# Optimization experiments

Measured on AMD Instinct MI355X. Metric: run time of the kernel, lower is better.

The kernel has to match this reference:

```python
import jax, jax.numpy as jnp
import numpy as np

PATCH_LEN = 16
PATCH_STRIDE = 8
DIM = 512
NUM_HEADS = 8
HEAD_DIM = DIM // NUM_HEADS
NUM_LAYERS = 4
MLP_HIDDEN = 4 * DIM
ROPE_BASE = 10000.0
LN_EPS = 1e-5


def setup_inputs() -> dict:
    key = jax.random.key(0)
    ks = jax.random.split(key, 20)
    B, T, C = 4, 8192, 7
    s = 0.02
    inp = {
        "x": jax.random.normal(ks[0], (B, T, C), dtype=jnp.float32),
        "W_emb": jax.random.normal(ks[1], (PATCH_LEN * C, DIM), dtype=jnp.float32) * s,
        "b_emb": jnp.zeros((DIM,), jnp.float32),
        "ln1_g": jnp.ones((NUM_LAYERS, DIM), jnp.float32),
        "ln1_b": jnp.zeros((NUM_LAYERS, DIM), jnp.float32),
        "W_qkv": jax.random.normal(ks[2], (NUM_LAYERS, DIM, 3 * DIM), dtype=jnp.float32) * s,
        "b_qkv": jnp.zeros((NUM_LAYERS, 3 * DIM), jnp.float32),
        "W_proj": jax.random.normal(ks[3], (NUM_LAYERS, DIM, DIM), dtype=jnp.float32) * s,
        "b_proj": jnp.zeros((NUM_LAYERS, DIM), jnp.float32),
        "ln2_g": jnp.ones((NUM_LAYERS, DIM), jnp.float32),
        "ln2_b": jnp.zeros((NUM_LAYERS, DIM), jnp.float32),
        "W_mlp1": jax.random.normal(ks[4], (NUM_LAYERS, DIM, MLP_HIDDEN), dtype=jnp.float32) * s,
        "b_mlp1": jnp.zeros((NUM_LAYERS, MLP_HIDDEN), jnp.float32),
        "W_mlp2": jax.random.normal(ks[5], (NUM_LAYERS, MLP_HIDDEN, DIM), dtype=jnp.float32) * s,
        "b_mlp2": jnp.zeros((NUM_LAYERS, DIM), jnp.float32),
        "lnf_g": jnp.ones((DIM,), jnp.float32),
        "lnf_b": jnp.zeros((DIM,), jnp.float32),
    }
    return inp


def _layer_norm(x, g, b):
    mu = jnp.mean(x, axis=-1, keepdims=True)
    var = jnp.mean(jnp.square(x - mu), axis=-1, keepdims=True)
    return (x - mu) * jax.lax.rsqrt(var + LN_EPS) * g + b


def _rotate_half(x):
    x1, x2 = jnp.split(x, 2, axis=-1)
    return jnp.concatenate((-x2, x1), axis=-1)


def _rope_cos_sin(seq_len):
    t = jnp.arange(seq_len, dtype=jnp.float32)
    inv_freq = 1.0 / (ROPE_BASE ** (jnp.arange(0, HEAD_DIM, 2, dtype=jnp.float32) / HEAD_DIM))
    freqs = jnp.outer(t, inv_freq)                      # [L, hd/2]
    emb = jnp.concatenate((freqs, freqs), axis=-1)      # [L, hd]
    return jnp.cos(emb), jnp.sin(emb)


def _forward(x, W_emb, b_emb, ln1_g, ln1_b, W_qkv, b_qkv, W_proj, b_proj,
             ln2_g, ln2_b, W_mlp1, b_mlp1, W_mlp2, b_mlp2, lnf_g, lnf_b):
    B, T, C = x.shape
    n = (T - PATCH_LEN) // PATCH_STRIDE + 1
    # torch unfold: [B, n, C, patch_len], then flattened as (C, patch_len)
    idx = jnp.arange(n)[:, None] * PATCH_STRIDE + jnp.arange(PATCH_LEN)[None, :]  # [n, P]
    patches = x[:, idx, :]                              # [B, n, P, C]
    patches = patches.transpose(0, 1, 3, 2).reshape(B, n, C * PATCH_LEN)
    emb = patches @ W_emb + b_emb                       # [B, n, D]

    cos, sin = _rope_cos_sin(n)                         # [n, hd]
    cos = cos[None, None, :, :]
    sin = sin[None, None, :, :]
    scale = HEAD_DIM ** -0.5

    h = emb
    for i in range(NUM_LAYERS):
        # --- attention ---
        y = _layer_norm(h, ln1_g[i], ln1_b[i])
        qkv = (y @ W_qkv[i] + b_qkv[i]).reshape(B, n, 3, NUM_HEADS, HEAD_DIM)
        qkv = qkv.transpose(2, 0, 3, 1, 4)              # [3, B, H, n, hd]
        q, k, v = qkv[0], qkv[1], qkv[2]
        q = q * cos + _rotate_half(q) * sin
        k = k * cos + _rotate_half(k) * sin
        attn = jax.nn.softmax(jnp.einsum('bhqd,bhkd->bhqk', q, k) * scale, axis=-1)
        o = jnp.einsum('bhqk,bhkd->bhqd', attn, v)      # [B, H, n, hd]
        o = o.transpose(0, 2, 1, 3).reshape(B, n, DIM)
        h = h + (o @ W_proj[i] + b_proj[i])
        # --- mlp ---
        y = _layer_norm(h, ln2_g[i], ln2_b[i])
        y = jax.nn.gelu(y @ W_mlp1[i] + b_mlp1[i], approximate=False)
        h = h + (y @ W_mlp2[i] + b_mlp2[i])

    x_out = _layer_norm(h, lnf_g, lnf_b)
    return emb, x_out


def reference(x, W_emb, b_emb, ln1_g, ln1_b, W_qkv, b_qkv, W_proj, b_proj,
              ln2_g, ln2_b, W_mlp1, b_mlp1, W_mlp2, b_mlp2, lnf_g, lnf_b):
    return _forward(x, W_emb, b_emb, ln1_g, ln1_b, W_qkv, b_qkv, W_proj, b_proj,
                    ln2_g, ln2_b, W_mlp1, b_mlp1, W_mlp2, b_mlp2, lnf_g, lnf_b)
```

## Files before the change

### kernel.cpp

```cpp
#include <hip/hip_runtime.h>
#include <hip/hip_bf16.h>
#include <math.h>

#define B_SZ 4
#define T_LEN 8192
#define C_IN 7
#define NPATCH 1023
#define DIM 512
#define NH 8
#define HD 64
#define NLAYERS 4
#define MLP_HID 2048
#define M_ROWS (B_SZ * NPATCH)
#define KEMB 128
#define LN_EPS 1e-5f

typedef __attribute__((ext_vector_type(8))) short short8;
typedef __attribute__((ext_vector_type(4))) float float4v;

static __device__ __forceinline__ unsigned short f2bf(float f) {
  __hip_bfloat16 h = __float2bfloat16(f);
  return *reinterpret_cast<unsigned short*>(&h);
}
static __device__ __forceinline__ float bf2f(unsigned short u) {
  return __uint_as_float(((unsigned)u) << 16);
}

__global__ __launch_bounds__(256) void patch_kernel(
    const float* __restrict__ x, unsigned short* __restrict__ Pm) {
  int idx = blockIdx.x * 256 + threadIdx.x;
  if (idx >= M_ROWS * KEMB) return;
  int row = idx >> 7, c = idx & 127;
  float v = 0.f;
  if (c < 112) {
    int b = row / NPATCH, i = row - b * NPATCH;
    int ci = c >> 4, p = c & 15;
    v = x[((size_t)b * T_LEN + (size_t)i * 8 + p) * C_IN + ci];
  }
  Pm[idx] = f2bf(v);
}

__global__ __launch_bounds__(256) void wemb_cvt_kernel(
    const float* __restrict__ W, unsigned short* __restrict__ Wt) {
  int idx = blockIdx.x * 256 + threadIdx.x;
  if (idx >= DIM * KEMB) return;
  int n = idx >> 7, k = idx & 127;
  float v = (k < 112) ? W[(size_t)k * DIM + n] : 0.f;
  Wt[idx] = f2bf(v);
}

template <bool BF>
__global__ __launch_bounds__(256) void ln_kernel(
    const float* __restrict__ in, const float* __restrict__ g,
    const float* __restrict__ bb, void* __restrict__ outv, int M) {
  int row = blockIdx.x * 4 + (threadIdx.x >> 6);
  if (row >= M) return;
  int lane = threadIdx.x & 63;
  const float* xr = in + (size_t)row * DIM;
  float v[8];
  float s = 0.f;
  #pragma unroll
  for (int k = 0; k < 8; ++k) { v[k] = xr[lane + 64 * k]; s += v[k]; }
  #pragma unroll
  for (int off = 32; off; off >>= 1) s += __shfl_down(s, off);
  s = __shfl(s, 0);
  float mu = s * (1.f / DIM);
  float q = 0.f;
  #pragma unroll
  for (int k = 0; k < 8; ++k) { float d = v[k] - mu; q = fmaf(d, d, q); }
  #pragma unroll
  for (int off = 32; off; off >>= 1) q += __shfl_down(q, off);
  q = __shfl(q, 0);
  float rstd = rsqrtf(q * (1.f / DIM) + LN_EPS);
  #pragma unroll
  for (int k = 0; k < 8; ++k) {
    int d = lane + 64 * k;
    float r = (v[k] - mu) * rstd * g[d] + bb[d];
    if (BF)
      ((unsigned short*)outv)[(size_t)row * DIM + d] = f2bf(r);
    else
      ((float*)outv)[(size_t)row * DIM + d] = r;
  }
}

__global__ __launch_bounds__(256) void wcvt_kernel(
    const float* __restrict__ W, unsigned short* __restrict__ Wt, int K, int N) {
  __shared__ float tile[32][33];
  int n0 = blockIdx.x * 32, k0 = blockIdx.y * 32, L = blockIdx.z;
  const float* Ws = W + (size_t)L * K * N;
  unsigned short* Wd = Wt + (size_t)L * K * N;
  int tx = threadIdx.x & 31, ty = threadIdx.x >> 5;
  #pragma unroll
  for (int i = 0; i < 4; ++i)
    tile[ty + i * 8][tx] = Ws[(size_t)(k0 + ty + i * 8) * N + n0 + tx];
  __syncthreads();
  #pragma unroll
  for (int i = 0; i < 4; ++i)
    Wd[(size_t)(n0 + ty + i * 8) * K + k0 + tx] = f2bf(tile[tx][ty + i * 8]);
}

__global__ __launch_bounds__(256) void rope_tab_kernel(float2* __restrict__ tab) {
  int idx = blockIdx.x * 256 + threadIdx.x;
  if (idx >= NPATCH * 32) return;
  int i = idx >> 5, j = idx & 31;
  float inv = powf(10000.0f, -(float)j * (1.0f / 32.0f));
  float sn, cs;
  sincosf((float)i * inv, &sn, &cs);
  tab[idx] = make_float2(cs, sn);
}

template <int TM, int TN, int EPI>
__global__ __launch_bounds__(256) void mfma_gemm(
    const unsigned short* __restrict__ A, const unsigned short* __restrict__ Bt,
    const float* __restrict__ bias, const float* __restrict__ res,
    float* __restrict__ Cf, float* __restrict__ Cf2,
    unsigned short* __restrict__ Cb, const float2* __restrict__ rtab,
    int M, int N, int K) {
  constexpr int WM = TM / 2, WN = TN / 2;
  constexpr int NI = WM / 16, NJ = WN / 16;
  constexpr int ACH = TM * 4;
  constexpr int TCH = (TM + TN) * 4;
  constexpr int CH = TCH / 256;
  __shared__ __align__(16) unsigned short As[2][TM][40];
  __shared__ __align__(16) unsigned short Bs[2][TN][40];
  const int bm = blockIdx.y * TM;
  const int bn = blockIdx.x * TN;
  const int tid = threadIdx.x;
  const int lane = tid & 63, wave = tid >> 6;
  const int quad = lane >> 4, l16 = lane & 15;
  const int wm = (wave & 1) * WM;
  const int wn = (wave >> 1) * WN;

  float4v acc[NI][NJ];
  #pragma unroll
  for (int i = 0; i < NI; ++i)
    #pragma unroll
    for (int j = 0; j < NJ; ++j)
      acc[i][j] = (float4v){0.f, 0.f, 0.f, 0.f};

  uint4 pr[CH];
  auto load_regs = [&](int kk) {
    #pragma unroll
    for (int it = 0; it < CH; ++it) {
      int c = tid + it * 256;
      if (c < ACH) {
        int row = c >> 2, ch = (c & 3) * 8;
        int gm = bm + row;
        pr[it] = make_uint4(0u, 0u, 0u, 0u);
        if (gm < M) pr[it] = *(const uint4*)(A + (size_t)gm * K + kk + ch);
      } else {
        int c2 = c - ACH;
        int row = c2 >> 2, ch = (c2 & 3) * 8;
        pr[it] = *(const uint4*)(Bt + (size_t)(bn + row) * K + kk + ch);
      }
    }
  };

  load_regs(0);
  int buf = 0;
  for (int k0 = 0; k0 < K; k0 += 32, buf ^= 1) {
    #pragma unroll
    for (int it = 0; it < CH; ++it) {
      int c = tid + it * 256;
      if (c < ACH)
        *(uint4*)&As[buf][c >> 2][(c & 3) * 8] = pr[it];
      else {
        int c2 = c - ACH;
        *(uint4*)&Bs[buf][c2 >> 2][(c2 & 3) * 8] = pr[it];
      }
    }
    if (k0 + 32 < K) load_regs(k0 + 32);
    __syncthreads();
    short8 af[NI], bfr[NJ];
    #pragma unroll
    for (int i = 0; i < NI; ++i)
      af[i] = *(const short8*)&As[buf][wm + i * 16 + l16][quad * 8];
    #pragma unroll
    for (int j = 0; j < NJ; ++j)
      bfr[j] = *(const short8*)&Bs[buf][wn + j * 16 + l16][quad * 8];
    #pragma unroll
    for (int i = 0; i < NI; ++i)
      #pragma unroll
      for (int j = 0; j < NJ; ++j)
        acc[i][j] = __builtin_amdgcn_mfma_f32_16x16x32_bf16(
            af[i], bfr[j], acc[i][j], 0, 0, 0);
  }

  if (EPI == 6) {
    const int sec = (bn + wn) >> 9;
    #pragma unroll
    for (int i = 0; i < NI; ++i) {
      int gm0 = bm + wm + i * 16 + quad * 4;
      #pragma unroll
      for (int r = 0; r < 4; ++r) {
        int gm = gm0 + r;
        if (gm >= M) continue;
        size_t rowoff = (size_t)gm * N;
        if (sec < 2) {
          int ip = gm; if (ip >= 2046) ip -= 2046; if (ip >= 1023) ip -= 1023;
          float sc = (sec == 0) ? 0.125f : 1.f;
          #pragma unroll
          for (int j = 0; j < 2; ++j) {
            int gn = bn + wn + j * 16 + l16;
            float v0 = acc[i][j][r] + bias[gn];
            float v1 = acc[i][j + 2][r] + bias[gn + 32];
            float2 t = rtab[ip * 32 + j * 16 + l16];
            Cb[rowoff + gn]      = f2bf((v0 * t.x - v1 * t.y) * sc);
            Cb[rowoff + gn + 32] = f2bf((v1 * t.x + v0 * t.y) * sc);
          }
        } else {
          #pragma unroll
          for (int j = 0; j < 4; ++j) {
            int gn = bn + wn + j * 16 + l16;
            Cb[rowoff + gn] = f2bf(acc[i][j][r] + bias[gn]);
          }
        }
      }
    }
    return;
  }

  #pragma unroll
  for (int j = 0; j < NJ; ++j) {
    int gn = bn + wn + j * 16 + l16;
    float bv = bias[gn];
    #pragma unroll
    for (int i = 0; i < NI; ++i) {
      int gm0 = bm + wm + i * 16 + quad * 4;
      #pragma unroll
      for (int r = 0; r < 4; ++r) {
        int gm = gm0 + r;
        if (gm < M) {
          float v = acc[i][j][r] + bv;
          size_t off = (size_t)gm * N + gn;
          if (EPI == 1) {
            Cf[off] = v + res[off];
          } else if (EPI == 2) {
            Cb[off] = f2bf(0.5f * v * (1.f + erff(v * 0.70710678118f)));
          } else if (EPI == 3) {
            Cb[off] = f2bf(v);
          } else {
            Cf[off] = v;
            Cf2[off] = v;
          }
        }
      }
    }
  }
}

#define APITCH 72

__global__ __launch_bounds__(256) void attn_kernel(
    const unsigned short* __restrict__ qkvb, unsigned short* __restrict__ o) {
  const int qt0 = blockIdx.x * 64;
  const int h = blockIdx.y;
  const int b = blockIdx.z;
  const int tid = threadIdx.x;
  const int lane = tid & 63, wave = tid >> 6;
  const int quad = lane >> 4, l16 = lane & 15;

  __shared__ __align__(16) unsigned short Qs[64][APITCH];
  __shared__ __align__(16) unsigned short Vt[2][HD][APITCH];
  __shared__ __align__(16) unsigned short Ps[4][16][APITCH];

  const int sr = tid >> 2;
  const int sc0 = (tid & 3) * 16;
  {
    int qi = qt0 + sr;
    uint4 a = make_uint4(0u, 0u, 0u, 0u), b2 = a;
    if (qi < NPATCH) {
      const uint4* src = (const uint4*)(qkvb + (size_t)(b * NPATCH + qi) * (3 * DIM) + h * HD + sc0);
      a = src[0]; b2 = src[1];
    }
    *(uint4*)&Qs[sr][sc0] = a;
    *(uint4*)&Qs[sr][sc0 + 8] = b2;
  }

  const int kp = tid & 31, dg = tid >> 5;
  uint4 pv0, pv1;
  auto load_v = [&](int j0) {
    pv0 = pv1 = make_uint4(0u, 0u, 0u, 0u);
    int j = j0 + 2 * kp;
    const unsigned short* vb = qkvb + (size_t)(b * NPATCH + j) * (3 * DIM) + 2 * DIM + h * HD + dg * 8;
    if (j < NPATCH)     pv0 = *(const uint4*)vb;
    if (j + 1 < NPATCH) pv1 = *(const uint4*)(vb + 3 * DIM);
  };

  const unsigned short* kbase = qkvb + (size_t)b * NPATCH * (3 * DIM) + DIM + (size_t)h * HD;
  uint4 nk0[4], nk1[4];
  auto load_k = [&](int j0) {
    #pragma unroll
    for (int j = 0; j < 4; ++j) {
      int row = j0 + j * 16 + l16;
      nk0[j] = make_uint4(0u, 0u, 0u, 0u);
      nk1[j] = nk0[j];
      if (row < NPATCH) {
        const uint4* kr = (const uint4*)(kbase + (size_t)row * (3 * DIM) + quad * 8);
        nk0[j] = kr[0];
        nk1[j] = kr[4];
      }
    }
  };

  load_v(0);
  load_k(0);
  __syncthreads();

  short8 aq0 = *(const short8*)&Qs[wave * 16 + l16][quad * 8];
  short8 aq1 = *(const short8*)&Qs[wave * 16 + l16][32 + quad * 8];

  float4v accO[4];
  #pragma unroll
  for (int j2 = 0; j2 < 4; ++j2) accO[j2] = (float4v){0.f, 0.f, 0.f, 0.f};
  float m_run[4] = {-1e30f, -1e30f, -1e30f, -1e30f};
  float lp[4] = {0.f, 0.f, 0.f, 0.f};

  int buf = 0;
  for (int j0 = 0; j0 < NPATCH; j0 += 64, buf ^= 1) {
    {
      unsigned short va[8], vb8[8];
      *(uint4*)&va[0] = pv0;
      *(uint4*)&vb8[0] = pv1;
      #pragma unroll
      for (int u = 0; u < 8; ++u) {
        unsigned pk = (unsigned)va[u] | ((unsigned)vb8[u] << 16);
        *(unsigned*)&Vt[buf][dg * 8 + u][2 * kp] = pk;
      }
    }
    __syncthreads();

    float4v s[4];
    __builtin_amdgcn_s_setprio(1);
    #pragma unroll
    for (int j = 0; j < 4; ++j) {
      s[j] = (float4v){0.f, 0.f, 0.f, 0.f};
      s[j] = __builtin_amdgcn_mfma_f32_16x16x32_bf16(
          aq0, __builtin_bit_cast(short8, nk0[j]), s[j], 0, 0, 0);
      s[j] = __builtin_amdgcn_mfma_f32_16x16x32_bf16(
          aq1, __builtin_bit_cast(short8, nk1[j]), s[j], 0, 0, 0);
    }
    __builtin_amdgcn_s_setprio(0);

    if (j0 + 64 < NPATCH) { load_k(j0 + 64); load_v(j0 + 64); }

    float mx[4];
    #pragma unroll
    for (int r = 0; r < 4; ++r)
      mx[r] = fmaxf(fmaxf(s[0][r], s[1][r]), fmaxf(s[2][r], s[3][r]));
    #pragma unroll
    for (int mask = 1; mask < 16; mask <<= 1)
      #pragma unroll
      for (int r = 0; r < 4; ++r)
        mx[r] = fmaxf(mx[r], __shfl_xor(mx[r], mask));
    float g = fmaxf(fmaxf(mx[0] - m_run[0], mx[1] - m_run[1]),
                    fmaxf(mx[2] - m_run[2], mx[3] - m_run[3]));
    if (!__all(g <= 8.f)) {
      #pragma unroll
      for (int r = 0; r < 4; ++r) {
        float mnew = fmaxf(m_run[r], mx[r]);
        float al = __expf(m_run[r] - mnew);
        m_run[r] = mnew;
        lp[r] *= al;
        #pragma unroll
        for (int j2 = 0; j2 < 4; ++j2) accO[j2][r] *= al;
      }
    }
    #pragma unroll
    for (int j = 0; j < 4; ++j) {
      bool valid = (j0 + j * 16 + l16) < NPATCH;
      #pragma unroll
      for (int r = 0; r < 4; ++r) {
        float p = valid ? __expf(s[j][r] - m_run[r]) : 0.f;
        lp[r] += p;
        Ps[wave][quad * 4 + r][j * 16 + l16] = f2bf(p);
      }
    }

    short8 pa0 = *(const short8*)&Ps[wave][l16][quad * 8];
    short8 pa1 = *(const short8*)&Ps[wave][l16][32 + quad * 8];
    __builtin_amdgcn_s_setprio(1);
    #pragma unroll
    for (int j2 = 0; j2 < 4; ++j2) {
      short8 v0 = *(const short8*)&Vt[buf][j2 * 16 + l16][quad * 8];
      short8 v1 = *(const short8*)&Vt[buf][j2 * 16 + l16][32 + quad * 8];
      accO[j2] = __builtin_amdgcn_mfma_f32_16x16x32_bf16(pa0, v0, accO[j2], 0, 0, 0);
      accO[j2] = __builtin_amdgcn_mfma_f32_16x16x32_bf16(pa1, v1, accO[j2], 0, 0, 0);
    }
    __builtin_amdgcn_s_setprio(0);
  }

  #pragma unroll
  for (int mask = 1; mask < 16; mask <<= 1)
    #pragma unroll
    for (int r = 0; r < 4; ++r)
      lp[r] += __shfl_xor(lp[r], mask);

  #pragma unroll
  for (int r = 0; r < 4; ++r) {
    int qi = qt0 + wave * 16 + quad * 4 + r;
    if (qi < NPATCH) {
      float inv = 1.f / lp[r];
      size_t off = (size_t)(b * NPATCH + qi) * DIM + h * HD + l16;
      #pragma unroll
      for (int j2 = 0; j2 < 4; ++j2)
        o[off + j2 * 16] = f2bf(accO[j2][r] * inv);
    }
  }
}

extern "C" void kernel_launch(void* const* d_in, const int* in_sizes, int n_in,
                              void* d_out, int out_size, void* d_ws, size_t ws_size,
                              hipStream_t stream) {
  const float* x      = (const float*)d_in[0];
  const float* W_emb  = (const float*)d_in[1];
  const float* b_emb  = (const float*)d_in[2];
  const float* ln1_g  = (const float*)d_in[3];
  const float* ln1_b  = (const float*)d_in[4];
  const float* W_qkv  = (const float*)d_in[5];
  const float* b_qkv  = (const float*)d_in[6];
  const float* W_proj = (const float*)d_in[7];
  const float* b_proj = (const float*)d_in[8];
  const float* ln2_g  = (const float*)d_in[9];
  const float* ln2_b  = (const float*)d_in[10];
  const float* W_mlp1 = (const float*)d_in[11];
  const float* b_mlp1 = (const float*)d_in[12];
  const float* W_mlp2 = (const float*)d_in[13];
  const float* b_mlp2 = (const float*)d_in[14];
  const float* lnf_g  = (const float*)d_in[15];
  const float* lnf_b  = (const float*)d_in[16];
  float* out = (float*)d_out;

  float* h              = (float*)d_ws;
  unsigned short* qkvb  = (unsigned short*)(h + (size_t)M_ROWS * DIM);
  unsigned short* midbf = qkvb;
  unsigned short* ybf   = qkvb + (size_t)M_ROWS * MLP_HID;
  unsigned short* obf   = ybf;
  unsigned short* wqkv_t  = ybf + (size_t)M_ROWS * DIM;
  unsigned short* wproj_t = wqkv_t  + (size_t)NLAYERS * DIM * 3 * DIM;
  unsigned short* wmlp1_t = wproj_t + (size_t)NLAYERS * DIM * DIM;
  unsigned short* wmlp2_t = wmlp1_t + (size_t)NLAYERS * DIM * MLP_HID;
  float2* rtab = (float2*)(wmlp2_t + (size_t)NLAYERS * MLP_HID * DIM);
  unsigned short* Pm    = (unsigned short*)(rtab + (size_t)NPATCH * 32);
  unsigned short* Wembt = Pm + (size_t)M_ROWS * KEMB;

  wcvt_kernel<<<dim3(3 * DIM / 32, DIM / 32, NLAYERS), 256, 0, stream>>>(W_qkv,  wqkv_t,  DIM, 3 * DIM);
  wcvt_kernel<<<dim3(DIM / 32, DIM / 32, NLAYERS),     256, 0, stream>>>(W_proj, wproj_t, DIM, DIM);
  wcvt_kernel<<<dim3(MLP_HID / 32, DIM / 32, NLAYERS), 256, 0, stream>>>(W_mlp1, wmlp1_t, DIM, MLP_HID);
  wcvt_kernel<<<dim3(DIM / 32, MLP_HID / 32, NLAYERS), 256, 0, stream>>>(W_mlp2, wmlp2_t, MLP_HID, DIM);
  rope_tab_kernel<<<(NPATCH * 32 + 255) / 256, 256, 0, stream>>>(rtab);
  patch_kernel<<<(M_ROWS * KEMB + 255) / 256, 256, 0, stream>>>(x, Pm);
  wemb_cvt_kernel<<<(DIM * KEMB + 255) / 256, 256, 0, stream>>>(W_emb, Wembt);

  const int MT64 = (M_ROWS + 63) / 64;
  const int LNG = (M_ROWS + 3) / 4;

  mfma_gemm<64, 64, 5><<<dim3(DIM / 64, MT64), 256, 0, stream>>>(
      Pm, Wembt, b_emb, nullptr, out, h, nullptr, nullptr, M_ROWS, DIM, KEMB);

  for (int L = 0; L < NLAYERS; ++L) {
    ln_kernel<true><<<LNG, 256, 0, stream>>>(h, ln1_g + L * DIM, ln1_b + L * DIM, ybf, M_ROWS);
    mfma_gemm<64, 128, 6><<<dim3(3 * DIM / 128, MT64), 256, 0, stream>>>(
        ybf, wqkv_t + (size_t)L * DIM * 3 * DIM, b_qkv + L * 3 * DIM,
        nullptr, nullptr, nullptr, qkvb, rtab, M_ROWS, 3 * DIM, DIM);
    attn_kernel<<<dim3((NPATCH + 63) / 64, NH, B_SZ), 256, 0, stream>>>(qkvb, obf);
    mfma_gemm<64, 64, 1><<<dim3(DIM / 64, MT64), 256, 0, stream>>>(
        obf, wproj_t + (size_t)L * DIM * DIM, b_proj + L * DIM,
        h, h, nullptr, nullptr, nullptr, M_ROWS, DIM, DIM);
    ln_kernel<true><<<LNG, 256, 0, stream>>>(h, ln2_g + L * DIM, ln2_b + L * DIM, ybf, M_ROWS);
    mfma_gemm<64, 128, 2><<<dim3(MLP_HID / 128, MT64), 256, 0, stream>>>(
        ybf, wmlp1_t + (size_t)L * DIM * MLP_HID, b_mlp1 + L * MLP_HID,
        nullptr, nullptr, nullptr, midbf, nullptr, M_ROWS, MLP_HID, DIM);
    mfma_gemm<64, 64, 1><<<dim3(DIM / 64, MT64), 256, 0, stream>>>(
        midbf, wmlp2_t + (size_t)L * MLP_HID * DIM, b_mlp2 + L * DIM,
        h, h, nullptr, nullptr, nullptr, M_ROWS, DIM, MLP_HID);
  }

  ln_kernel<false><<<LNG, 256, 0, stream>>>(h, lnf_g, lnf_b, out + (size_t)M_ROWS * DIM, M_ROWS);
}
```

Measured before the change: 712.4 us.

## Stage K through LDS, remap attention grid per XCD, enlarge QKV/MLP1 GEMM tiles

Attention K tiles are now loaded cooperatively into a double-buffered LDS array, replacing per-lane strided register fetches, and the prefetch of the next K/V tile is issued before the QK MFMAs. The attention grid becomes a flat 512-block launch that maps each (batch, head) to a single XCD so its K/V rows stay in that die's L2. The QKV and MLP1 GEMMs switch from 64x128 to 128x128 tiles, which halves the block count, and the GEMM MFMA loop gets raised wave priority. The larger tiles raise register and LDS use and cut the number of blocks available for parallelism.

Result: faster. 692.9 us (-2.7%).

```diff
diff --git a/kernel.cpp b/kernel.cpp
--- a/kernel.cpp
+++ b/kernel.cpp
@@ -178,12 +178,14 @@
     #pragma unroll
     for (int j = 0; j < NJ; ++j)
       bfr[j] = *(const short8*)&Bs[buf][wn + j * 16 + l16][quad * 8];
+    __builtin_amdgcn_s_setprio(1);
     #pragma unroll
     for (int i = 0; i < NI; ++i)
       #pragma unroll
       for (int j = 0; j < NJ; ++j)
         acc[i][j] = __builtin_amdgcn_mfma_f32_16x16x32_bf16(
             af[i], bfr[j], acc[i][j], 0, 0, 0);
+    __builtin_amdgcn_s_setprio(0);
   }
 
   if (EPI == 6) {
@@ -200,17 +202,17 @@
           int ip = gm; if (ip >= 2046) ip -= 2046; if (ip >= 1023) ip -= 1023;
           float sc = (sec == 0) ? 0.125f : 1.f;
           #pragma unroll
-          for (int j = 0; j < 2; ++j) {
+          for (int j = 0; j < NJ / 2; ++j) {
             int gn = bn + wn + j * 16 + l16;
             float v0 = acc[i][j][r] + bias[gn];
-            float v1 = acc[i][j + 2][r] + bias[gn + 32];
+            float v1 = acc[i][j + NJ / 2][r] + bias[gn + 32];
             float2 t = rtab[ip * 32 + j * 16 + l16];
             Cb[rowoff + gn]      = f2bf((v0 * t.x - v1 * t.y) * sc);
             Cb[rowoff + gn + 32] = f2bf((v1 * t.x + v0 * t.y) * sc);
           }
         } else {
           #pragma unroll
-          for (int j = 0; j < 4; ++j) {
+          for (int j = 0; j < NJ; ++j) {
             int gn = bn + wn + j * 16 + l16;
             Cb[rowoff + gn] = f2bf(acc[i][j][r] + bias[gn]);
           }
@@ -253,19 +255,24 @@
 
 __global__ __launch_bounds__(256) void attn_kernel(
     const unsigned short* __restrict__ qkvb, unsigned short* __restrict__ o) {
-  const int qt0 = blockIdx.x * 64;
-  const int h = blockIdx.y;
-  const int b = blockIdx.z;
+  const int bid = blockIdx.x;
+  const int xcd = bid & 7, slot = bid >> 3;
+  const int qt0 = (slot & 15) * 64;
+  const int gh = xcd + 8 * (slot >> 4);
+  const int h = gh & 7, b = gh >> 3;
+
   const int tid = threadIdx.x;
   const int lane = tid & 63, wave = tid >> 6;
   const int quad = lane >> 4, l16 = lane & 15;
 
   __shared__ __align__(16) unsigned short Qs[64][APITCH];
+  __shared__ __align__(16) unsigned short Ks[2][64][APITCH];
   __shared__ __align__(16) unsigned short Vt[2][HD][APITCH];
   __shared__ __align__(16) unsigned short Ps[4][16][APITCH];
 
   const int sr = tid >> 2;
   const int sc0 = (tid & 3) * 16;
+
   {
     int qi = qt0 + sr;
     uint4 a = make_uint4(0u, 0u, 0u, 0u), b2 = a;
@@ -276,6 +283,17 @@
     *(uint4*)&Qs[sr][sc0] = a;
     *(uint4*)&Qs[sr][sc0 + 8] = b2;
   }
+
+  uint4 pk0, pk1;
+  auto load_k = [&](int j0) {
+    pk0 = pk1 = make_uint4(0u, 0u, 0u, 0u);
+    int j = j0 + sr;
+    if (j < NPATCH) {
+      const unsigned short* kb = qkvb + (size_t)(b * NPATCH + j) * (3 * DIM) + DIM + h * HD;
+      pk0 = *(const uint4*)(kb + sc0);
+      pk1 = *(const uint4*)(kb + sc0 + 8);
+    }
+  };
 
   const int kp = tid & 31, dg = tid >> 5;
   uint4 pv0, pv1;
@@ -287,24 +305,8 @@
     if (j + 1 < NPATCH) pv1 = *(const uint4*)(vb + 3 * DIM);
   };
 
-  const unsigned short* kbase = qkvb + (size_t)b * NPATCH * (3 * DIM) + DIM + (size_t)h * HD;
-  uint4 nk0[4], nk1[4];
-  auto load_k = [&](int j0) {
-    #pragma unroll
-    for (int j = 0; j < 4; ++j) {
-      int row = j0 + j * 16 + l16;
-      nk0[j] = make_uint4(0u, 0u, 0u, 0u);
-      nk1[j] = nk0[j];
-      if (row < NPATCH) {
-        const uint4* kr = (const uint4*)(kbase + (size_t)row * (3 * DIM) + quad * 8);
-        nk0[j] = kr[0];
-        nk1[j] = kr[4];
-      }
-    }
-  };
-
+  load_k(0);
   load_v(0);
-  load_k(0);
   __syncthreads();
 
   short8 aq0 = *(const short8*)&Qs[wave * 16 + l16][quad * 8];
@@ -319,6 +321,8 @@
   int buf = 0;
   for (int j0 = 0; j0 < NPATCH; j0 += 64, buf ^= 1) {
     {
+      *(uint4*)&Ks[buf][sr][sc0] = pk0;
+      *(uint4*)&Ks[buf][sr][sc0 + 8] = pk1;
       unsigned short va[8], vb8[8];
       *(uint4*)&va[0] = pv0;
       *(uint4*)&vb8[0] = pv1;
@@ -330,19 +334,19 @@
     }
     __syncthreads();
 
+    if (j0 + 64 < NPATCH) { load_k(j0 + 64); load_v(j0 + 64); }
+
     float4v s[4];
     __builtin_amdgcn_s_setprio(1);
     #pragma unroll
     for (int j = 0; j < 4; ++j) {
       s[j] = (float4v){0.f, 0.f, 0.f, 0.f};
-      s[j] = __builtin_amdgcn_mfma_f32_16x16x32_bf16(
-          aq0, __builtin_bit_cast(short8, nk0[j]), s[j], 0, 0, 0);
-      s[j] = __builtin_amdgcn_mfma_f32_16x16x32_bf16(
-          aq1, __builtin_bit_cast(short8, nk1[j]), s[j], 0, 0, 0);
+      short8 bk0 = *(const short8*)&Ks[buf][j * 16 + l16][quad * 8];
+      short8 bk1 = *(const short8*)&Ks[buf][j * 16 + l16][32 + quad * 8];
+      s[j] = __builtin_amdgcn_mfma_f32_16x16x32_bf16(aq0, bk0, s[j], 0, 0, 0);
+      s[j] = __builtin_amdgcn_mfma_f32_16x16x32_bf16(aq1, bk1, s[j], 0, 0, 0);
     }
     __builtin_amdgcn_s_setprio(0);
-
-    if (j0 + 64 < NPATCH) { load_k(j0 + 64); load_v(j0 + 64); }
 
     float mx[4];
     #pragma unroll
@@ -353,9 +357,9 @@
       #pragma unroll
       for (int r = 0; r < 4; ++r)
         mx[r] = fmaxf(mx[r], __shfl_xor(mx[r], mask));
-    float g = fmaxf(fmaxf(mx[0] - m_run[0], mx[1] - m_run[1]),
-                    fmaxf(mx[2] - m_run[2], mx[3] - m_run[3]));
-    if (!__all(g <= 8.f)) {
+    float gmax = fmaxf(fmaxf(mx[0] - m_run[0], mx[1] - m_run[1]),
+                       fmaxf(mx[2] - m_run[2], mx[3] - m_run[3]));
+    if (!__all(gmax <= 8.f)) {
       #pragma unroll
       for (int r = 0; r < 4; ++r) {
         float mnew = fmaxf(m_run[r], mx[r]);
@@ -453,6 +457,7 @@
   wemb_cvt_kernel<<<(DIM * KEMB + 255) / 256, 256, 0, stream>>>(W_emb, Wembt);
 
   const int MT64 = (M_ROWS + 63) / 64;
+  const int MT128 = (M_ROWS + 127) / 128;
   const int LNG = (M_ROWS + 3) / 4;
 
   mfma_gemm<64, 64, 5><<<dim3(DIM / 64, MT64), 256, 0, stream>>>(
@@ -460,15 +465,15 @@
 
   for (int L = 0; L < NLAYERS; ++L) {
     ln_kernel<true><<<LNG, 256, 0, stream>>>(h, ln1_g + L * DIM, ln1_b + L * DIM, ybf, M_ROWS);
-    mfma_gemm<64, 128, 6><<<dim3(3 * DIM / 128, MT64), 256, 0, stream>>>(
+    mfma_gemm<128, 128, 6><<<dim3(3 * DIM / 128, MT128), 256, 0, stream>>>(
         ybf, wqkv_t + (size_t)L * DIM * 3 * DIM, b_qkv + L * 3 * DIM,
         nullptr, nullptr, nullptr, qkvb, rtab, M_ROWS, 3 * DIM, DIM);
-    attn_kernel<<<dim3((NPATCH + 63) / 64, NH, B_SZ), 256, 0, stream>>>(qkvb, obf);
+    attn_kernel<<<dim3(512), 256, 0, stream>>>(qkvb, obf);
     mfma_gemm<64, 64, 1><<<dim3(DIM / 64, MT64), 256, 0, stream>>>(
         obf, wproj_t + (size_t)L * DIM * DIM, b_proj + L * DIM,
         h, h, nullptr, nullptr, nullptr, M_ROWS, DIM, DIM);
     ln_kernel<true><<<LNG, 256, 0, stream>>>(h, ln2_g + L * DIM, ln2_b + L * DIM, ybf, M_ROWS);
-    mfma_gemm<64, 128, 2><<<dim3(MLP_HID / 128, MT64), 256, 0, stream>>>(
+    mfma_gemm<128, 128, 2><<<dim3(MLP_HID / 128, MT128), 256, 0, stream>>>(
         ybf, wmlp1_t + (size_t)L * DIM * MLP_HID, b_mlp1 + L * MLP_HID,
         nullptr, nullptr, nullptr, midbf, nullptr, M_ROWS, MLP_HID, DIM);
     mfma_gemm<64, 64, 1><<<dim3(DIM / 64, MT64), 256, 0, stream>>>(
```
